# Kernel tuning notes

Measured on AMD Instinct MI355X. Metric: run time of the kernel, lower is better.

## Reference

```python
import jax, jax.numpy as jnp
import numpy as np

B, IN, F, HID, D, RH, OUT, C, R = 4096, 1024, 512, 128, 128, 64, 1, 10, 16


def setup_inputs() -> dict:
    key = jax.random.key(0)
    ks = jax.random.split(key, 24)
    def p(k, shape, s=0.05):
        return jax.random.normal(k, shape, jnp.float32) * s
    return {
        'x': jax.random.normal(ks[0], (B, IN), jnp.float32),
        'pref': jax.random.uniform(ks[1], (R, 2), jnp.float32),
        'base_w': p(ks[2], (F, IN)), 'base_b': p(ks[3], (F,)),
        'wm1_w': p(ks[4], (16, 2)), 'wm1_b': p(ks[5], (16,)),
        'wm2_w': p(ks[6], (C, 16)), 'wm2_b': p(ks[7], (C,)),
        'ray0_w': p(ks[8], (C, RH, 2)), 'ray0_b': p(ks[9], (C, RH)),
        'ray2_w': p(ks[10], (C, D, RH)), 'ray2_b': p(ks[11], (C, D)),
        'fc1_w': p(ks[12], (C, HID * F, D)), 'fc1_b': p(ks[13], (C, HID * F)),
        'b1_w': p(ks[14], (C, HID, D)), 'b1_b': p(ks[15], (C, HID)),
        'fc2_w': p(ks[16], (C, OUT * HID, D)), 'fc2_b': p(ks[17], (C, OUT * HID)),
        'b2_w': p(ks[18], (C, OUT, D)), 'b2_b': p(ks[19], (C, OUT)),
    }


def reference(x, pref, base_w, base_b, wm1_w, wm1_b, wm2_w, wm2_b,
              ray0_w, ray0_b, ray2_w, ray2_b, fc1_w, fc1_b,
              b1_w, b1_b, fc2_w, fc2_b, b2_w, b2_b):
    # base feature extractor: (B, F)
    feature = x @ base_w.T + base_b
    # client mixing weights per ray: (R, C), normalized over clients
    h = jax.nn.relu(pref @ wm1_w.T + wm1_b)
    w = jax.nn.sigmoid(h @ wm2_w.T + wm2_b)
    w = w / jnp.sum(w, axis=1, keepdims=True)
    # merged ray-MLP (nonlinear -> merge the tiny weights explicitly per ray)
    m0w = jnp.einsum('rc,cod->rod', w, ray0_w)          # (R, RH, 2)
    r1 = jax.nn.relu(jnp.einsum('rd,rod->ro', pref, m0w) + w @ ray0_b)
    m2w = jnp.einsum('rc,coh->roh', w, ray2_w)          # (R, D, RH)
    ray2v = jnp.einsum('rh,roh->ro', r1, m2w) + w @ ray2_b  # (R, D)

    def hyper(Wc, bc):
        # sum_c w[r,c] * (ray2v[r] @ Wc[c].T + bc[c])  == F.linear with merged params
        per_client = jnp.einsum('rd,cod->rco', ray2v, Wc)   # (R, C, O)
        return jnp.einsum('rc,rco->ro', w, per_client) + w @ bc

    W1 = hyper(fc1_w, fc1_b).reshape(R, HID, F)   # generated layer-1 weight
    b1 = hyper(b1_w, b1_b)                        # (R, HID)
    W2 = hyper(fc2_w, fc2_b).reshape(R, OUT, HID) # generated layer-2 weight
    b2 = hyper(b2_w, b2_b)                        # (R, OUT)

    v1 = jnp.einsum('bf,rhf->rbh', feature, W1) + b1[:, None, :]  # (R, B, HID)
    out = jnp.einsum('rbh,roh->rbo', v1, W2) + b2[:, None, :]     # (R, B, OUT)
    return jax.nn.sigmoid(out), out
```

## Files before the change

kernel.cpp:

```cpp
#include <hip/hip_runtime.h>
#include <cstddef>
#include <cstdint>


#define WS_WT    0
#define WS_RV    160
#define WS_W2T   2208
#define WS_WEFF  4256
#define WS_WFIN  12448
#define WS_BFIN  28832
#define WS_ZERO_BEG WS_RV
#define WS_ZERO_CNT (WS_BFIN + 16 - WS_RV)

__device__ __forceinline__ void front_mlp(const float* __restrict__ pref,
                                          const float* __restrict__ wm1_w,
                                          const float* __restrict__ wm1_b,
                                          const float* __restrict__ wm2_w,
                                          const float* __restrict__ wm2_b,
                                          float (*sh1)[16], float (*sw)[10],
                                          float* sinv) {
  const int t = threadIdx.x;
  {
    int r = t >> 4, j = t & 15;
    float v = pref[r * 2 + 0] * wm1_w[j * 2 + 0] + pref[r * 2 + 1] * wm1_w[j * 2 + 1] + wm1_b[j];
    sh1[r][j] = fmaxf(v, 0.f);
  }
  __syncthreads();
  if (t < 160) {
    int r = t / 10, c = t % 10;
    float z = wm2_b[c];
    for (int j = 0; j < 16; ++j) z += sh1[r][j] * wm2_w[c * 16 + j];
    sw[r][c] = 1.f / (1.f + expf(-z));
  }
  __syncthreads();
  if (t < 16) {
    float s = 0.f;
    for (int c = 0; c < 10; ++c) s += sw[t][c];
    sinv[t] = 1.f / s;
  }
  __syncthreads();
  if (t < 160) {
    int r = t / 10, c = t % 10;
    sw[r][c] = sw[r][c] * sinv[r];
  }
  __syncthreads();
}

__global__ __launch_bounds__(256) void k_stage1(
    const float* __restrict__ pref, const float* __restrict__ wm1_w,
    const float* __restrict__ wm1_b, const float* __restrict__ wm2_w,
    const float* __restrict__ wm2_b, const float* __restrict__ ray0_w,
    const float* __restrict__ ray0_b, const float* __restrict__ ray2_w,
    const float* __restrict__ ray2_b, const float* __restrict__ fc2_b,
    float* __restrict__ ws) {
  __shared__ float sh1[16][16];
  __shared__ float sw[16][10];
  __shared__ float sinv[16];
  __shared__ float r1s[16][65];
  const int t = threadIdx.x;
  front_mlp(pref, wm1_w, wm1_b, wm2_w, wm2_b, sh1, sw, sinv);
  for (int it = t; it < 1024; it += 256) {
    int r = it >> 6, o = it & 63;
    float m0 = 0.f, m1 = 0.f, rb = 0.f;
    for (int c = 0; c < 10; ++c) {
      float wv = sw[r][c];
      m0 += wv * ray0_w[(c * 64 + o) * 2 + 0];
      m1 += wv * ray0_w[(c * 64 + o) * 2 + 1];
      rb += wv * ray0_b[c * 64 + o];
    }
    float v = pref[r * 2 + 0] * m0 + pref[r * 2 + 1] * m1 + rb;
    r1s[r][o] = fmaxf(v, 0.f);
  }
  __syncthreads();
  const int pair = blockIdx.x * 16 + (t >> 4);
  const int r = t & 15;
  const float* row = ray2_w + (size_t)pair * 64;
  const float* r1r = r1s[r];
  float dot = 0.f;
#pragma unroll
  for (int k = 0; k < 64; ++k) dot += row[k] * r1r[k];
  int c = pair >> 7, d = pair & 127;
  atomicAdd(&ws[WS_RV + r * 128 + d], sw[r][c] * dot);

  if (blockIdx.x == 0) {
    if (t < 160) ws[WS_WT + t] = sw[t & 15][t >> 4];
    for (int i = t; i < 2048; i += 256) {
      int rr = i >> 7, dd = i & 127;
      float s = 0.f;
      for (int cc = 0; cc < 10; ++cc) s += sw[rr][cc] * ray2_b[cc * 128 + dd];
      atomicAdd(&ws[WS_RV + i], s);
    }
  } else if (blockIdx.x == 1) {
    for (int i = t; i < 2048; i += 256) {
      int h = i >> 4, rr = i & 15;
      float s = 0.f;
      for (int cc = 0; cc < 10; ++cc) s += sw[rr][cc] * fc2_b[cc * 128 + h];
      atomicAdd(&ws[WS_W2T + i], s);
    }
  }
}

__global__ __launch_bounds__(256) void k_stage2(const float* __restrict__ fc2_w,
                                                float* __restrict__ ws) {
  const int t = threadIdx.x;
  const int lane = t & 63;
  const int wv = blockIdx.x * 4 + (t >> 6);
  float2 rv2[16];
#pragma unroll
  for (int r = 0; r < 16; ++r) rv2[r] = *(const float2*)&ws[WS_RV + r * 128 + lane * 2];
  for (int q = 0; q < 4; ++q) {
    int rid = wv * 4 + q;
    int c = rid >> 7, h = rid & 127;
    float2 a = *(const float2*)&fc2_w[(size_t)rid * 128 + lane * 2];
    float u[16];
#pragma unroll
    for (int r = 0; r < 16; ++r) u[r] = a.x * rv2[r].x + a.y * rv2[r].y;
#pragma unroll
    for (int m = 1; m <= 32; m <<= 1) {
#pragma unroll
      for (int r = 0; r < 16; ++r) u[r] += __shfl_xor(u[r], m, 64);
    }
    if (lane == 0) {
#pragma unroll
      for (int r = 0; r < 16; ++r)
        atomicAdd(&ws[WS_W2T + h * 16 + r], u[r] * ws[WS_WT + c * 16 + r]);
    }
  }
}

__global__ __launch_bounds__(256, 3) void k_main(
    const float* __restrict__ fc1_w, const float* __restrict__ fc1_b,
    const float* __restrict__ b1_w, const float* __restrict__ b1_b,
    const float* __restrict__ b2_w, const float* __restrict__ b2_b,
    float* __restrict__ ws) {
  __shared__ float scoef[2560];
  __shared__ float bfred[4][16];
  const int blk = blockIdx.x;
  const int t = threadIdx.x;

  if (blk < 2048) {
    const int wid = t >> 6, lane = t & 63, l32 = lane & 31;
    const int ch0 = (blk >> 6) * 40;
    const int fp = (blk & 63) * 4 + wid;
    for (int i = t; i < 640; i += 256) {
      int chl = i >> 4, r = i & 15;
      int ch = ch0 + chl, c = ch >> 7, h = ch & 127;
      scoef[i] = ws[WS_WT + c * 16 + r] * ws[WS_W2T + h * 16 + r];
    }
    float4 rv[16];
#pragma unroll
    for (int r = 0; r < 16; ++r) rv[r] = *(const float4*)&ws[WS_RV + r * 128 + l32 * 4];
    __syncthreads();

    float acc[16];
#pragma unroll
    for (int r = 0; r < 16; ++r) acc[r] = 0.f;

    const float4* p = (const float4*)fc1_w + (size_t)ch0 * 16384 + fp * 64 + lane;

    float4 buf[8];
#pragma unroll
    for (int j = 0; j < 8; ++j) buf[j] = p[(size_t)j * 16384];

    for (int g = 0; g < 5; ++g) {
#pragma unroll
      for (int k = 0; k < 8; ++k) {
        const int chl = g * 8 + k;
        float4 cur = buf[k];
        int nxt = chl + 8; if (nxt > 39) nxt = 39;
        buf[k] = p[(size_t)nxt * 16384];
        const float4* cf = (const float4*)(scoef + chl * 16);
        float4 c0 = cf[0], c1 = cf[1], c2 = cf[2], c3 = cf[3];
        float cw[16] = {c0.x, c0.y, c0.z, c0.w, c1.x, c1.y, c1.z, c1.w,
                        c2.x, c2.y, c2.z, c2.w, c3.x, c3.y, c3.z, c3.w};
#pragma unroll
        for (int r = 0; r < 16; ++r) {
          float tt = cur.x * rv[r].x + cur.y * rv[r].y + cur.z * rv[r].z + cur.w * rv[r].w;
          acc[r] = fmaf(cw[r], tt, acc[r]);
        }
      }
    }

#pragma unroll
    for (int m = 1; m <= 16; m <<= 1) {
#pragma unroll
      for (int r = 0; r < 16; ++r) acc[r] += __shfl_xor(acc[r], m, 64);
    }
    if (l32 == 0) {
      const int f = fp * 2 + (lane >> 5);
#pragma unroll
      for (int r = 0; r < 16; ++r) atomicAdd(&ws[WS_WEFF + r * 512 + f], acc[r]);
    }
  } else if (blk < 2064) {
    const int bb = blk - 2048;
    const int f = (bb & 1) * 256 + t;
    const int ch0 = (bb >> 1) * 160;
    for (int i = t; i < 2560; i += 256) {
      int chl = i >> 4, r = i & 15;
      int ch = ch0 + chl, c = ch >> 7, h = ch & 127;
      scoef[i] = ws[WS_WT + c * 16 + r] * ws[WS_W2T + h * 16 + r];
    }
    __syncthreads();
    float acc[16];
#pragma unroll
    for (int r = 0; r < 16; ++r) acc[r] = 0.f;
    const float* q = fc1_b + (size_t)ch0 * 512 + f;
    float b4[4];
#pragma unroll
    for (int j = 0; j < 4; ++j) b4[j] = q[(size_t)j * 512];
    for (int g = 0; g < 40; ++g) {
#pragma unroll
      for (int k = 0; k < 4; ++k) {
        const int it = g * 4 + k;
        float xv = b4[k];
        int nxt = it + 4; if (nxt > 159) nxt = 159;
        b4[k] = q[(size_t)nxt * 512];
        const float4* cf = (const float4*)(scoef + it * 16);
        float4 c0 = cf[0], c1 = cf[1], c2 = cf[2], c3 = cf[3];
        float cw[16] = {c0.x, c0.y, c0.z, c0.w, c1.x, c1.y, c1.z, c1.w,
                        c2.x, c2.y, c2.z, c2.w, c3.x, c3.y, c3.z, c3.w};
#pragma unroll
        for (int r = 0; r < 16; ++r) acc[r] = fmaf(cw[r], xv, acc[r]);
      }
    }
#pragma unroll
    for (int r = 0; r < 16; ++r) atomicAdd(&ws[WS_WEFF + r * 512 + f], acc[r]);
  } else if (blk < 2072) {
    const int hb = blk - 2064;
    const int wid = t >> 6, lane = t & 63;
    const int ch0b = hb * 160;
    for (int i = t; i < 2560; i += 256) {
      int chl = i >> 4, r = i & 15;
      int ch = ch0b + chl, c = ch >> 7, h = ch & 127;
      scoef[i] = ws[WS_WT + c * 16 + r] * ws[WS_W2T + h * 16 + r];
    }
    __syncthreads();
    float2 rv2[16];
#pragma unroll
    for (int r = 0; r < 16; ++r) rv2[r] = *(const float2*)&ws[WS_RV + r * 128 + lane * 2];
    float acc[16];
#pragma unroll
    for (int r = 0; r < 16; ++r) acc[r] = 0.f;
    const int chl0 = wid * 40;
    const float2* q = (const float2*)b1_w + (size_t)(ch0b + chl0) * 64 + lane;
    float2 b2buf[4];
#pragma unroll
    for (int j = 0; j < 4; ++j) b2buf[j] = q[(size_t)j * 64];
    for (int g = 0; g < 10; ++g) {
#pragma unroll
      for (int k = 0; k < 4; ++k) {
        const int it = g * 4 + k;
        float2 cur = b2buf[k];
        int nxt = it + 4; if (nxt > 39) nxt = 39;
        b2buf[k] = q[(size_t)nxt * 64];
        const float4* cf = (const float4*)(scoef + (chl0 + it) * 16);
        float4 c0 = cf[0], c1 = cf[1], c2 = cf[2], c3 = cf[3];
        float cw[16] = {c0.x, c0.y, c0.z, c0.w, c1.x, c1.y, c1.z, c1.w,
                        c2.x, c2.y, c2.z, c2.w, c3.x, c3.y, c3.z, c3.w};
#pragma unroll
        for (int r = 0; r < 16; ++r)
          acc[r] = fmaf(cw[r], cur.x * rv2[r].x + cur.y * rv2[r].y, acc[r]);
      }
    }
#pragma unroll
    for (int m = 1; m <= 32; m <<= 1) {
#pragma unroll
      for (int r = 0; r < 16; ++r) acc[r] += __shfl_xor(acc[r], m, 64);
    }
    if (lane == 0) {
#pragma unroll
      for (int r = 0; r < 16; ++r) bfred[wid][r] = acc[r];
    }
    __syncthreads();
    if (t < 16)
      atomicAdd(&ws[WS_BFIN + t], bfred[0][t] + bfred[1][t] + bfred[2][t] + bfred[3][t]);
  } else {
    const int wid = t >> 6, lane = t & 63;
    float acc[16];
#pragma unroll
    for (int r = 0; r < 16; ++r) acc[r] = 0.f;
    for (int i = t; i < 1280; i += 256) {
      int c = i >> 7, h = i & 127;
      float v = b1_b[c * 128 + h];
#pragma unroll
      for (int r = 0; r < 16; ++r)
        acc[r] = fmaf(ws[WS_WT + c * 16 + r] * ws[WS_W2T + h * 16 + r], v, acc[r]);
    }
    for (int i = t; i < 1280; i += 256) {
      int c = i >> 7, d = i & 127;
      float v = b2_w[c * 128 + d];
#pragma unroll
      for (int r = 0; r < 16; ++r)
        acc[r] = fmaf(ws[WS_WT + c * 16 + r] * ws[WS_RV + r * 128 + d], v, acc[r]);
    }
    if (t < 10) {
      float v = b2_b[t];
#pragma unroll
      for (int r = 0; r < 16; ++r) acc[r] = fmaf(ws[WS_WT + t * 16 + r], v, acc[r]);
    }
#pragma unroll
    for (int m = 1; m <= 32; m <<= 1) {
#pragma unroll
      for (int r = 0; r < 16; ++r) acc[r] += __shfl_xor(acc[r], m, 64);
    }
    if (lane == 0) {
#pragma unroll
      for (int r = 0; r < 16; ++r) bfred[wid][r] = acc[r];
    }
    __syncthreads();
    if (t < 16)
      atomicAdd(&ws[WS_BFIN + t], bfred[0][t] + bfred[1][t] + bfred[2][t] + bfred[3][t]);
  }
}

__global__ __launch_bounds__(256) void k_wfin(const float* __restrict__ base_w,
                                              const float* __restrict__ base_b,
                                              float* __restrict__ ws) {
  const int t = threadIdx.x;
  const int blk = blockIdx.x;
  const int i = (blk & 3) * 256 + t;
  const int f0 = (blk >> 2) * 16;
  const float* WEFF = ws + WS_WEFF;
  float acc[16];
#pragma unroll
  for (int r = 0; r < 16; ++r) acc[r] = 0.f;
#pragma unroll 4
  for (int f = f0; f < f0 + 16; ++f) {
    float bw = base_w[(size_t)f * 1024 + i];
#pragma unroll
    for (int r = 0; r < 16; ++r) acc[r] = fmaf(WEFF[r * 512 + f], bw, acc[r]);
  }
#pragma unroll
  for (int r = 0; r < 16; ++r) atomicAdd(&ws[WS_WFIN + r * 1024 + i], acc[r]);

  if (blk == 0 && t < 64) {
    float a2[16];
#pragma unroll
    for (int r = 0; r < 16; ++r) a2[r] = 0.f;
    for (int f = t; f < 512; f += 64) {
      float v = base_b[f];
#pragma unroll
      for (int r = 0; r < 16; ++r) a2[r] = fmaf(WEFF[r * 512 + f], v, a2[r]);
    }
#pragma unroll
    for (int m = 1; m <= 32; m <<= 1) {
#pragma unroll
      for (int r = 0; r < 16; ++r) a2[r] += __shfl_xor(a2[r], m, 64);
    }
    if (t == 0) {
#pragma unroll
      for (int r = 0; r < 16; ++r) atomicAdd(&ws[WS_BFIN + r], a2[r]);
    }
  }
}

__global__ __launch_bounds__(256) void k_out(const float* __restrict__ x,
                                             const float* __restrict__ ws,
                                             float* __restrict__ out) {
  __shared__ float4 wfs[4096];
  const int t = threadIdx.x;
  const float4* wf4 = (const float4*)(ws + WS_WFIN);
#pragma unroll
  for (int k = 0; k < 16; ++k) wfs[t + 256 * k] = wf4[t + 256 * k];
  __syncthreads();

  const int b0 = blockIdx.x * 16;
  const int bp = t >> 5;
  const int isub = t & 31;
  const int bA = b0 + bp * 2;
  const float* xa = x + (size_t)bA * 1024;
  const float* xb = xa + 1024;
  float acc0[16], acc1[16];
#pragma unroll
  for (int r = 0; r < 16; ++r) { acc0[r] = 0.f; acc1[r] = 0.f; }

  for (int chunk = 0; chunk < 4; ++chunk) {
#pragma unroll
    for (int j = 0; j < 2; ++j) {
      const int off = chunk * 256 + j * 128 + isub * 4;
      float4 xv0 = *(const float4*)&xa[off];
      float4 xv1 = *(const float4*)&xb[off];
      const float4* wrow = wfs + chunk * 64 + j * 32 + isub;
#pragma unroll
      for (int r = 0; r < 16; ++r) {
        float4 w = wrow[r * 256];
        acc0[r] += xv0.x * w.x + xv0.y * w.y + xv0.z * w.z + xv0.w * w.w;
        acc1[r] += xv1.x * w.x + xv1.y * w.y + xv1.z * w.z + xv1.w * w.w;
      }
    }
  }
#pragma unroll
  for (int m = 1; m <= 16; m <<= 1) {
#pragma unroll
    for (int r = 0; r < 16; ++r) {
      acc0[r] += __shfl_xor(acc0[r], m, 64);
      acc1[r] += __shfl_xor(acc1[r], m, 64);
    }
  }
  if (isub == 0) {
#pragma unroll
    for (int r = 0; r < 16; ++r) {
      float bf = ws[WS_BFIN + r];
      float v0 = acc0[r] + bf;
      float v1 = acc1[r] + bf;
      out[r * 4096 + bA] = 1.f / (1.f + expf(-v0));
      out[r * 4096 + bA + 1] = 1.f / (1.f + expf(-v1));
      out[65536 + r * 4096 + bA] = v0;
      out[65536 + r * 4096 + bA + 1] = v1;
    }
  }
}

extern "C" void kernel_launch(void* const* d_in, const int* in_sizes, int n_in,
                              void* d_out, int out_size, void* d_ws, size_t ws_size,
                              hipStream_t stream) {
  (void)in_sizes; (void)n_in; (void)out_size; (void)ws_size;
  const float* x      = (const float*)d_in[0];
  const float* pref   = (const float*)d_in[1];
  const float* base_w = (const float*)d_in[2];
  const float* base_b = (const float*)d_in[3];
  const float* wm1_w  = (const float*)d_in[4];
  const float* wm1_b  = (const float*)d_in[5];
  const float* wm2_w  = (const float*)d_in[6];
  const float* wm2_b  = (const float*)d_in[7];
  const float* ray0_w = (const float*)d_in[8];
  const float* ray0_b = (const float*)d_in[9];
  const float* ray2_w = (const float*)d_in[10];
  const float* ray2_b = (const float*)d_in[11];
  const float* fc1_w  = (const float*)d_in[12];
  const float* fc1_b  = (const float*)d_in[13];
  const float* b1_w   = (const float*)d_in[14];
  const float* b1_b   = (const float*)d_in[15];
  const float* fc2_w  = (const float*)d_in[16];
  const float* fc2_b  = (const float*)d_in[17];
  const float* b2_w   = (const float*)d_in[18];
  const float* b2_b   = (const float*)d_in[19];
  float* ws  = (float*)d_ws;
  float* out = (float*)d_out;

  hipMemsetAsync(ws + WS_ZERO_BEG, 0, (size_t)WS_ZERO_CNT * sizeof(float), stream);
  k_stage1<<<80, 256, 0, stream>>>(pref, wm1_w, wm1_b, wm2_w, wm2_b,
                                   ray0_w, ray0_b, ray2_w, ray2_b, fc2_b, ws);
  k_stage2<<<80, 256, 0, stream>>>(fc2_w, ws);
  k_main<<<2073, 256, 0, stream>>>(fc1_w, fc1_b, b1_w, b1_b, b2_w, b2_b, ws);
  k_wfin<<<128, 256, 0, stream>>>(base_w, base_b, ws);
  k_out<<<256, 256, 0, stream>>>(x, ws, out);
}
```

Baseline: 557.1 us.

## Fuse all stages into one persistent cooperative kernel with grid syncs

Replaces the memset and five separate kernel launches with a single cooperative kernel of 512 blocks that runs each stage in turn, separated by grid-wide syncs. The point is to cut launch overhead and the idle gaps between dependent stages, and the old path is kept as a fallback if a cooperative launch is unavailable. The big fc1 streaming stage now runs on 512 blocks instead of 2073, and 64KB of LDS per block may limit occupancy. Each grid.sync also adds its own cost.

```diff
diff --git a/kernel.cpp b/kernel.cpp
--- a/kernel.cpp
+++ b/kernel.cpp
@@ -1,4 +1,5 @@
 #include <hip/hip_runtime.h>
+#include <hip/hip_cooperative_groups.h>
 #include <cstddef>
 #include <cstdint>
 
@@ -11,6 +12,417 @@
 #define WS_BFIN  28832
 #define WS_ZERO_BEG WS_RV
 #define WS_ZERO_CNT (WS_BFIN + 16 - WS_RV)
+
+namespace cg = cooperative_groups;
+
+__device__ __forceinline__ void front_mlp_flat(const float* __restrict__ pref,
+                                               const float* __restrict__ wm1_w,
+                                               const float* __restrict__ wm1_b,
+                                               const float* __restrict__ wm2_w,
+                                               const float* __restrict__ wm2_b,
+                                               float* sh1, float* sw, float* sinv) {
+  const int t = threadIdx.x;
+  {
+    int r = t >> 4, j = t & 15;
+    float v = pref[r * 2 + 0] * wm1_w[j * 2 + 0] + pref[r * 2 + 1] * wm1_w[j * 2 + 1] + wm1_b[j];
+    sh1[r * 16 + j] = fmaxf(v, 0.f);
+  }
+  __syncthreads();
+  if (t < 160) {
+    int r = t / 10, c = t % 10;
+    float z = wm2_b[c];
+    for (int j = 0; j < 16; ++j) z += sh1[r * 16 + j] * wm2_w[c * 16 + j];
+    sw[r * 10 + c] = 1.f / (1.f + expf(-z));
+  }
+  __syncthreads();
+  if (t < 16) {
+    float s = 0.f;
+    for (int c = 0; c < 10; ++c) s += sw[t * 10 + c];
+    sinv[t] = 1.f / s;
+  }
+  __syncthreads();
+  if (t < 160) {
+    int r = t / 10, c = t % 10;
+    sw[r * 10 + c] = sw[r * 10 + c] * sinv[r];
+  }
+  __syncthreads();
+}
+
+__global__ __launch_bounds__(256, 2) void k_all(
+    const float* __restrict__ x, const float* __restrict__ pref,
+    const float* __restrict__ base_w, const float* __restrict__ base_b,
+    const float* __restrict__ wm1_w, const float* __restrict__ wm1_b,
+    const float* __restrict__ wm2_w, const float* __restrict__ wm2_b,
+    const float* __restrict__ ray0_w, const float* __restrict__ ray0_b,
+    const float* __restrict__ ray2_w, const float* __restrict__ ray2_b,
+    const float* __restrict__ fc1_w, const float* __restrict__ fc1_b,
+    const float* __restrict__ b1_w, const float* __restrict__ b1_b,
+    const float* __restrict__ fc2_w, const float* __restrict__ fc2_b,
+    const float* __restrict__ b2_w, const float* __restrict__ b2_b,
+    float* __restrict__ ws, float* __restrict__ out) {
+  __shared__ float4 sm4[4096];
+  float* smf = (float*)sm4;
+  cg::grid_group grid = cg::this_grid();
+  const int t = threadIdx.x;
+  const int blk = blockIdx.x;
+  const int gid = blk * 256 + t;
+
+  if (gid < 12288) ws[WS_RV + gid] = 0.f;
+  else if (gid < 12304) ws[WS_BFIN + (gid - 12288)] = 0.f;
+  grid.sync();
+
+  if (blk < 80) {
+    float* sh1  = smf;
+    float* sw   = smf + 256;
+    float* sinv = smf + 416;
+    float* r1s  = smf + 432;
+    front_mlp_flat(pref, wm1_w, wm1_b, wm2_w, wm2_b, sh1, sw, sinv);
+    for (int it = t; it < 1024; it += 256) {
+      int r = it >> 6, o = it & 63;
+      float m0 = 0.f, m1 = 0.f, rb = 0.f;
+      for (int c = 0; c < 10; ++c) {
+        float wv = sw[r * 10 + c];
+        m0 += wv * ray0_w[(c * 64 + o) * 2 + 0];
+        m1 += wv * ray0_w[(c * 64 + o) * 2 + 1];
+        rb += wv * ray0_b[c * 64 + o];
+      }
+      float v = pref[r * 2 + 0] * m0 + pref[r * 2 + 1] * m1 + rb;
+      r1s[r * 65 + o] = fmaxf(v, 0.f);
+    }
+    __syncthreads();
+    const int pair = blk * 16 + (t >> 4);
+    const int r = t & 15;
+    const float* row = ray2_w + (size_t)pair * 64;
+    const float* r1r = r1s + r * 65;
+    float dot = 0.f;
+#pragma unroll
+    for (int k = 0; k < 64; ++k) dot += row[k] * r1r[k];
+    int c = pair >> 7, d = pair & 127;
+    atomicAdd(&ws[WS_RV + r * 128 + d], sw[r * 10 + c] * dot);
+
+    if (blk == 0) {
+      if (t < 160) ws[WS_WT + t] = sw[(t & 15) * 10 + (t >> 4)];
+      for (int i = t; i < 2048; i += 256) {
+        int rr = i >> 7, dd = i & 127;
+        float s = 0.f;
+        for (int cc = 0; cc < 10; ++cc) s += sw[rr * 10 + cc] * ray2_b[cc * 128 + dd];
+        atomicAdd(&ws[WS_RV + i], s);
+      }
+    } else if (blk == 1) {
+      for (int i = t; i < 2048; i += 256) {
+        int h = i >> 4, rr = i & 15;
+        float s = 0.f;
+        for (int cc = 0; cc < 10; ++cc) s += sw[rr * 10 + cc] * fc2_b[cc * 128 + h];
+        atomicAdd(&ws[WS_W2T + i], s);
+      }
+    }
+  }
+  grid.sync();
+
+  {
+    const int wid = t >> 6, lane = t & 63;
+    const int rid = blk * 4 + wid;
+    if (rid < 1280) {
+      float2 rvl[16];
+#pragma unroll
+      for (int r = 0; r < 16; ++r) rvl[r] = *(const float2*)&ws[WS_RV + r * 128 + lane * 2];
+      float2 a = *(const float2*)&fc2_w[(size_t)rid * 128 + lane * 2];
+      float u[16];
+#pragma unroll
+      for (int r = 0; r < 16; ++r) u[r] = a.x * rvl[r].x + a.y * rvl[r].y;
+#pragma unroll
+      for (int m = 1; m <= 32; m <<= 1) {
+#pragma unroll
+        for (int r = 0; r < 16; ++r) u[r] += __shfl_xor(u[r], m, 64);
+      }
+      if (lane == 0) {
+        int c = rid >> 7, h = rid & 127;
+#pragma unroll
+        for (int r = 0; r < 16; ++r)
+          atomicAdd(&ws[WS_W2T + h * 16 + r], u[r] * ws[WS_WT + c * 16 + r]);
+      }
+    }
+  }
+  grid.sync();
+
+  {
+    float* scoef = smf;
+    float* bfred = smf + 2560;
+    const int wid = t >> 6, lane = t & 63, l32 = lane & 31;
+    const int ch0 = (blk >> 6) * 160;
+    const int fp  = (blk & 63) * 4 + wid;
+    for (int i = t; i < 2560; i += 256) {
+      int chl = i >> 4, r = i & 15;
+      int ch = ch0 + chl, c = ch >> 7, h = ch & 127;
+      scoef[i] = ws[WS_WT + c * 16 + r] * ws[WS_W2T + h * 16 + r];
+    }
+    float4 rv[16];
+#pragma unroll
+    for (int r = 0; r < 16; ++r) rv[r] = *(const float4*)&ws[WS_RV + r * 128 + l32 * 4];
+    __syncthreads();
+
+    float acc[16];
+#pragma unroll
+    for (int r = 0; r < 16; ++r) acc[r] = 0.f;
+
+    const float4* p = (const float4*)fc1_w + (size_t)ch0 * 16384 + fp * 64 + lane;
+    float4 buf[8];
+#pragma unroll
+    for (int j = 0; j < 8; ++j) buf[j] = p[(size_t)j * 16384];
+
+    for (int g = 0; g < 20; ++g) {
+#pragma unroll
+      for (int k = 0; k < 8; ++k) {
+        const int chl = g * 8 + k;
+        float4 cur = buf[k];
+        int nxt = chl + 8; if (nxt > 159) nxt = 159;
+        buf[k] = p[(size_t)nxt * 16384];
+        const float4* cf = (const float4*)(scoef + chl * 16);
+        float4 c0 = cf[0], c1 = cf[1], c2 = cf[2], c3 = cf[3];
+        float cw[16] = {c0.x, c0.y, c0.z, c0.w, c1.x, c1.y, c1.z, c1.w,
+                        c2.x, c2.y, c2.z, c2.w, c3.x, c3.y, c3.z, c3.w};
+#pragma unroll
+        for (int r = 0; r < 16; ++r) {
+          float tt = cur.x * rv[r].x + cur.y * rv[r].y + cur.z * rv[r].z + cur.w * rv[r].w;
+          acc[r] = fmaf(cw[r], tt, acc[r]);
+        }
+      }
+    }
+#pragma unroll
+    for (int m = 1; m <= 16; m <<= 1) {
+#pragma unroll
+      for (int r = 0; r < 16; ++r) acc[r] += __shfl_xor(acc[r], m, 64);
+    }
+    if (l32 == 0) {
+      const int f = fp * 2 + (lane >> 5);
+#pragma unroll
+      for (int r = 0; r < 16; ++r) atomicAdd(&ws[WS_WEFF + r * 512 + f], acc[r]);
+    }
+    __syncthreads();
+
+    if (blk < 16) {
+      const int bb = blk;
+      const int f = (bb & 1) * 256 + t;
+      const int ch0b = (bb >> 1) * 160;
+      for (int i = t; i < 2560; i += 256) {
+        int chl = i >> 4, r = i & 15;
+        int ch = ch0b + chl, c = ch >> 7, h = ch & 127;
+        scoef[i] = ws[WS_WT + c * 16 + r] * ws[WS_W2T + h * 16 + r];
+      }
+      __syncthreads();
+      float a2[16];
+#pragma unroll
+      for (int r = 0; r < 16; ++r) a2[r] = 0.f;
+      const float* q = fc1_b + (size_t)ch0b * 512 + f;
+      float b4[4];
+#pragma unroll
+      for (int j = 0; j < 4; ++j) b4[j] = q[(size_t)j * 512];
+      for (int g = 0; g < 40; ++g) {
+#pragma unroll
+        for (int k = 0; k < 4; ++k) {
+          const int it = g * 4 + k;
+          float xv = b4[k];
+          int nxt = it + 4; if (nxt > 159) nxt = 159;
+          b4[k] = q[(size_t)nxt * 512];
+          const float4* cf = (const float4*)(scoef + it * 16);
+          float4 c0 = cf[0], c1 = cf[1], c2 = cf[2], c3 = cf[3];
+          float cw[16] = {c0.x, c0.y, c0.z, c0.w, c1.x, c1.y, c1.z, c1.w,
+                          c2.x, c2.y, c2.z, c2.w, c3.x, c3.y, c3.z, c3.w};
+#pragma unroll
+          for (int r = 0; r < 16; ++r) a2[r] = fmaf(cw[r], xv, a2[r]);
+        }
+      }
+#pragma unroll
+      for (int r = 0; r < 16; ++r) atomicAdd(&ws[WS_WEFF + r * 512 + f], a2[r]);
+    } else if (blk < 24) {
+      const int hb = blk - 16;
+      const int ch0b = hb * 160;
+      for (int i = t; i < 2560; i += 256) {
+        int chl = i >> 4, r = i & 15;
+        int ch = ch0b + chl, c = ch >> 7, h = ch & 127;
+        scoef[i] = ws[WS_WT + c * 16 + r] * ws[WS_W2T + h * 16 + r];
+      }
+      __syncthreads();
+      float2 rv2[16];
+#pragma unroll
+      for (int r = 0; r < 16; ++r) rv2[r] = *(const float2*)&ws[WS_RV + r * 128 + lane * 2];
+      float a2[16];
+#pragma unroll
+      for (int r = 0; r < 16; ++r) a2[r] = 0.f;
+      const int chl0 = wid * 40;
+      const float2* q = (const float2*)b1_w + (size_t)(ch0b + chl0) * 64 + lane;
+      float2 b2buf[4];
+#pragma unroll
+      for (int j = 0; j < 4; ++j) b2buf[j] = q[(size_t)j * 64];
+      for (int g = 0; g < 10; ++g) {
+#pragma unroll
+        for (int k = 0; k < 4; ++k) {
+          const int it = g * 4 + k;
+          float2 cur = b2buf[k];
+          int nxt = it + 4; if (nxt > 39) nxt = 39;
+          b2buf[k] = q[(size_t)nxt * 64];
+          const float4* cf = (const float4*)(scoef + (chl0 + it) * 16);
+          float4 c0 = cf[0], c1 = cf[1], c2 = cf[2], c3 = cf[3];
+          float cw[16] = {c0.x, c0.y, c0.z, c0.w, c1.x, c1.y, c1.z, c1.w,
+                          c2.x, c2.y, c2.z, c2.w, c3.x, c3.y, c3.z, c3.w};
+#pragma unroll
+          for (int r = 0; r < 16; ++r)
+            a2[r] = fmaf(cw[r], cur.x * rv2[r].x + cur.y * rv2[r].y, a2[r]);
+        }
+      }
+#pragma unroll
+      for (int m = 1; m <= 32; m <<= 1) {
+#pragma unroll
+        for (int r = 0; r < 16; ++r) a2[r] += __shfl_xor(a2[r], m, 64);
+      }
+      if (lane == 0) {
+#pragma unroll
+        for (int r = 0; r < 16; ++r) bfred[wid * 16 + r] = a2[r];
+      }
+      __syncthreads();
+      if (t < 16)
+        atomicAdd(&ws[WS_BFIN + t], bfred[t] + bfred[16 + t] + bfred[32 + t] + bfred[48 + t]);
+    } else if (blk == 24) {
+      float a2[16];
+#pragma unroll
+      for (int r = 0; r < 16; ++r) a2[r] = 0.f;
+      for (int i = t; i < 1280; i += 256) {
+        int c = i >> 7, h = i & 127;
+        float v = b1_b[c * 128 + h];
+#pragma unroll
+        for (int r = 0; r < 16; ++r)
+          a2[r] = fmaf(ws[WS_WT + c * 16 + r] * ws[WS_W2T + h * 16 + r], v, a2[r]);
+      }
+      for (int i = t; i < 1280; i += 256) {
+        int c = i >> 7, d = i & 127;
+        float v = b2_w[c * 128 + d];
+#pragma unroll
+        for (int r = 0; r < 16; ++r)
+          a2[r] = fmaf(ws[WS_WT + c * 16 + r] * ws[WS_RV + r * 128 + d], v, a2[r]);
+      }
+      if (t < 10) {
+        float v = b2_b[t];
+#pragma unroll
+        for (int r = 0; r < 16; ++r) a2[r] = fmaf(ws[WS_WT + t * 16 + r], v, a2[r]);
+      }
+#pragma unroll
+      for (int m = 1; m <= 32; m <<= 1) {
+#pragma unroll
+        for (int r = 0; r < 16; ++r) a2[r] += __shfl_xor(a2[r], m, 64);
+      }
+      if (lane == 0) {
+#pragma unroll
+        for (int r = 0; r < 16; ++r) bfred[wid * 16 + r] = a2[r];
+      }
+      __syncthreads();
+      if (t < 16)
+        atomicAdd(&ws[WS_BFIN + t], bfred[t] + bfred[16 + t] + bfred[32 + t] + bfred[48 + t]);
+    }
+  }
+  grid.sync();
+
+  if (blk < 32) {
+    const int il = t & 31, fg = t >> 5;
+    const int i = blk * 32 + il;
+    const float* WEFF = ws + WS_WEFF;
+    float a4[16];
+#pragma unroll
+    for (int r = 0; r < 16; ++r) a4[r] = 0.f;
+    const int f0 = fg * 64;
+    for (int f = f0; f < f0 + 64; ++f) {
+      float bw = base_w[(size_t)f * 1024 + i];
+#pragma unroll
+      for (int r = 0; r < 16; ++r) a4[r] = fmaf(WEFF[r * 512 + f], bw, a4[r]);
+    }
+    float* red = smf;
+#pragma unroll
+    for (int r = 0; r < 16; ++r) red[fg * 512 + il * 16 + r] = a4[r];
+    __syncthreads();
+    for (int o = t; o < 512; o += 256) {
+      int ir = o >> 4, r = o & 15;
+      float s = 0.f;
+#pragma unroll
+      for (int fg2 = 0; fg2 < 8; ++fg2) s += red[fg2 * 512 + ir * 16 + r];
+      ws[WS_WFIN + r * 1024 + blk * 32 + ir] = s;
+    }
+  } else if (blk == 32) {
+    if (t < 64) {
+      const float* WEFF = ws + WS_WEFF;
+      float a2[16];
+#pragma unroll
+      for (int r = 0; r < 16; ++r) a2[r] = 0.f;
+      for (int f = t; f < 512; f += 64) {
+        float v = base_b[f];
+#pragma unroll
+        for (int r = 0; r < 16; ++r) a2[r] = fmaf(WEFF[r * 512 + f], v, a2[r]);
+      }
+#pragma unroll
+      for (int m = 1; m <= 32; m <<= 1) {
+#pragma unroll
+        for (int r = 0; r < 16; ++r) a2[r] += __shfl_xor(a2[r], m, 64);
+      }
+      if (t == 0) {
+#pragma unroll
+        for (int r = 0; r < 16; ++r) atomicAdd(&ws[WS_BFIN + r], a2[r]);
+      }
+    }
+  }
+  grid.sync();
+
+  if (blk < 256) {
+    float4* wfs = sm4;
+    const float4* wf4 = (const float4*)(ws + WS_WFIN);
+#pragma unroll
+    for (int k = 0; k < 16; ++k) wfs[t + 256 * k] = wf4[t + 256 * k];
+    __syncthreads();
+
+    const int b0 = blk * 16;
+    const int bp = t >> 5;
+    const int isub = t & 31;
+    const int bA = b0 + bp * 2;
+    const float* xa = x + (size_t)bA * 1024;
+    const float* xb = xa + 1024;
+    float acc0[16], acc1[16];
+#pragma unroll
+    for (int r = 0; r < 16; ++r) { acc0[r] = 0.f; acc1[r] = 0.f; }
+
+    for (int chunk = 0; chunk < 4; ++chunk) {
+#pragma unroll
+      for (int j = 0; j < 2; ++j) {
+        const int off = chunk * 256 + j * 128 + isub * 4;
+        float4 xv0 = *(const float4*)&xa[off];
+        float4 xv1 = *(const float4*)&xb[off];
+        const float4* wrow = wfs + chunk * 64 + j * 32 + isub;
+#pragma unroll
+        for (int r = 0; r < 16; ++r) {
+          float4 w = wrow[r * 256];
+          acc0[r] += xv0.x * w.x + xv0.y * w.y + xv0.z * w.z + xv0.w * w.w;
+          acc1[r] += xv1.x * w.x + xv1.y * w.y + xv1.z * w.z + xv1.w * w.w;
+        }
+      }
+    }
+#pragma unroll
+    for (int m = 1; m <= 16; m <<= 1) {
+#pragma unroll
+      for (int r = 0; r < 16; ++r) {
+        acc0[r] += __shfl_xor(acc0[r], m, 64);
+        acc1[r] += __shfl_xor(acc1[r], m, 64);
+      }
+    }
+    if (isub == 0) {
+#pragma unroll
+      for (int r = 0; r < 16; ++r) {
+        float bf = ws[WS_BFIN + r];
+        float v0 = acc0[r] + bf;
+        float v1 = acc1[r] + bf;
+        out[r * 4096 + bA] = 1.f / (1.f + expf(-v0));
+        out[r * 4096 + bA + 1] = 1.f / (1.f + expf(-v1));
+        out[65536 + r * 4096 + bA] = v0;
+        out[65536 + r * 4096 + bA + 1] = v1;
+      }
+    }
+  }
+}
 
 __device__ __forceinline__ void front_mlp(const float* __restrict__ pref,
                                           const float* __restrict__ wm1_w,
@@ -438,6 +850,29 @@
   float* ws  = (float*)d_ws;
   float* out = (float*)d_out;
 
+  static int g_mode = -1;
+  if (g_mode < 0) {
+    int maxb = 0;
+    hipError_t e1 = hipOccupancyMaxActiveBlocksPerMultiprocessor(&maxb, k_all, 256, 0);
+    int coop = 0, dev = 0;
+    (void)hipGetDevice(&dev);
+    hipError_t e2 = hipDeviceGetAttribute(&coop, hipDeviceAttributeCooperativeLaunch, dev);
+    g_mode = (e1 == hipSuccess && maxb >= 2 && (e2 != hipSuccess || coop != 0)) ? 1 : 0;
+  }
+
+  if (g_mode == 1) {
+    void* args[] = {
+        (void*)&x, (void*)&pref, (void*)&base_w, (void*)&base_b,
+        (void*)&wm1_w, (void*)&wm1_b, (void*)&wm2_w, (void*)&wm2_b,
+        (void*)&ray0_w, (void*)&ray0_b, (void*)&ray2_w, (void*)&ray2_b,
+        (void*)&fc1_w, (void*)&fc1_b, (void*)&b1_w, (void*)&b1_b,
+        (void*)&fc2_w, (void*)&fc2_b, (void*)&b2_w, (void*)&b2_b,
+        (void*)&ws, (void*)&out};
+    hipError_t e = hipLaunchCooperativeKernel(k_all, dim3(512), dim3(256), args, 0, stream);
+    if (e == hipSuccess) return;
+    g_mode = 0;
+  }
+
   hipMemsetAsync(ws + WS_ZERO_BEG, 0, (size_t)WS_ZERO_CNT * sizeof(float), stream);
   k_stage1<<<80, 256, 0, stream>>>(pref, wm1_w, wm1_b, wm2_w, wm2_b,
                                    ray0_w, ray0_b, ray2_w, ray2_b, fc2_b, ws);
```

Measured after the change: 557.9 us. About the same (+0.1%).
